# Optimization experiments

Hardware: AMD Instinct MI355X
Metric: run time of the kernel (lower is better)

The kernel has to match this reference:

```python
import jax, jax.numpy as jnp
import numpy as np

B = 256; SEED = 120; PRED = 24; D = 126; H = 1024
J = 14; JD = 9; HEADS = 4; DH = H // HEADS; SPLH = 128
PARENTS = (-1, -1, 0, 1, 2, 3, -1, 6, -1, -1, 8, 9, 10, 11)  # sparse SPL kinematic tree


def setup_inputs() -> dict:
    key = jax.random.key(0)
    ks = jax.random.split(key, 18)
    s = 0.02
    w = lambda k, shape: jax.random.normal(k, shape, dtype=jnp.float32) * s
    return {
        "poses": jax.random.normal(ks[0], (B, SEED + PRED, D), dtype=jnp.float32),
        "gru_Wih": w(ks[1], (3 * H, D)), "gru_Whh": w(ks[2], (3 * H, H)),
        "gru_bih": w(ks[3], (3 * H,)), "gru_bhh": w(ks[4], (3 * H,)),
        "pre_W": w(ks[5], (H, H)), "pre_b": w(ks[6], (H,)),
        "fp_W": w(ks[7], (H, D)), "fp_b": w(ks[8], (H,)),
        "inproj_W": w(ks[9], (3 * H, H)), "inproj_b": w(ks[10], (3 * H,)),
        "outproj_W": w(ks[11], (H, H)), "outproj_b": w(ks[12], (H,)),
        # per-joint SPL MLPs, stacked; root joints see zero-padded parent slot
        "spl_W1": w(ks[13], (J, SPLH, H + JD)), "spl_b1": w(ks[14], (J, SPLH)),
        "spl_W2": w(ks[15], (J, JD, SPLH)), "spl_b2": w(ks[16], (J, JD)),
    }


def _gru_cell(x, h, Wih, Whh, bih, bhh):
    gi = x @ Wih.T + bih
    gh = h @ Whh.T + bhh
    ir, iz, inn = jnp.split(gi, 3, axis=-1)
    hr, hz, hn = jnp.split(gh, 3, axis=-1)
    r = jax.nn.sigmoid(ir + hr)
    z = jax.nn.sigmoid(iz + hz)
    n = jnp.tanh(inn + r * hn)
    return (1.0 - z) * n + z * h


def _forward(poses, gru_Wih, gru_Whh, gru_bih, gru_bhh, pre_W, pre_b,
             fp_W, fp_b, inproj_W, inproj_b, outproj_W, outproj_b,
             spl_W1, spl_b1, spl_W2, spl_b2):
    input_seq = poses[:, :SEED]  # (B, T_in, D)
    # --- DCT motion attention (rFFT proxy) ---
    freq = jnp.fft.rfft(input_seq, axis=1).real          # (B, F, D), F = SEED//2+1
    feat = freq @ fp_W.T + fp_b                          # (B, F, H)
    qkv = feat @ inproj_W.T + inproj_b
    q, k, v = jnp.split(qkv, 3, axis=-1)
    hsplit = lambda t: t.reshape(t.shape[0], t.shape[1], HEADS, DH)
    q, k, v = hsplit(q), hsplit(k), hsplit(v)
    att = jax.nn.softmax(jnp.einsum('bqhd,bkhd->bhqk', q, k) / np.sqrt(DH).astype(np.float32), axis=-1)
    ctx = jnp.einsum('bhqk,bkhd->bqhd', att, v).reshape(feat.shape)
    attn_out = ctx @ outproj_W.T + outproj_b
    motion_ctx = attn_out.mean(axis=1)                   # (B, H)
    # --- GRU encode over seed ---
    h0 = jnp.zeros((poses.shape[0], H), dtype=poses.dtype)
    def enc(h, x):
        return _gru_cell(x, h, gru_Wih, gru_Whh, gru_bih, gru_bhh), None
    h, _ = jax.lax.scan(enc, h0, jnp.swapaxes(input_seq, 0, 1))
    x_last = input_seq[:, -1]
    # --- hierarchical SPL (sparse mode) ---
    def spl(hid):
        zero = jnp.zeros((hid.shape[0], JD), dtype=hid.dtype)
        preds = [None] * J
        for j in range(J):
            p = PARENTS[j]
            par = zero if p == -1 else preds[p]
            inp = jnp.concatenate([hid, par], axis=-1)   # (B, H+JD)
            hh = jax.nn.relu(inp @ spl_W1[j].T + spl_b1[j])
            preds[j] = jnp.tanh(hh @ spl_W2[j].T + spl_b2[j])
        return jnp.concatenate(preds, axis=-1)            # (B, J*JD)
    def dec(carry, _):
        x, hc = carry
        hc = _gru_cell(x, hc, gru_Wih, gru_Whh, gru_bih, gru_bhh)
        hid = jax.nn.relu(hc @ pre_W.T + pre_b) + motion_ctx
        x = x + spl(hid)
        return (x, hc), x
    _, ys = jax.lax.scan(dec, (x_last, h), None, length=PRED)
    return jnp.swapaxes(ys, 0, 1)                         # (B, PRED, D)


def reference(poses, gru_Wih, gru_Whh, gru_bih, gru_bhh, pre_W, pre_b,
              fp_W, fp_b, inproj_W, inproj_b, outproj_W, outproj_b,
              spl_W1, spl_b1, spl_W2, spl_b2):
    return _forward(poses, gru_Wih, gru_Whh, gru_bih, gru_bhh, pre_W, pre_b,
                    fp_W, fp_b, inproj_W, inproj_b, outproj_W, outproj_b,
                    spl_W1, spl_b1, spl_W2, spl_b2)
```

## Files before the change

kernel.cpp:

```cpp
#include <hip/hip_runtime.h>
#include <hip/hip_bf16.h>

typedef __hip_bfloat16 bf16;
typedef __attribute__((ext_vector_type(8))) short v8bf;
typedef __attribute__((ext_vector_type(16))) float f32x16;
typedef __attribute__((ext_vector_type(4))) float f32x4;
typedef unsigned long long ull;

#define B_    256
#define SEED_ 120
#define PRED_ 24
#define D_    126
#define H_    1024
#define F_    61
#define HEADS_ 4
#define DH_   256

#define GLD16(lds, g) __builtin_amdgcn_global_load_lds( \
    (const __attribute__((address_space(1))) unsigned int*)(g), \
    (__attribute__((address_space(3))) unsigned int*)(lds), 16, 0, 0)
#define VMWAIT(n) asm volatile("s_waitcnt vmcnt(" #n ")" ::: "memory")
#define BARRIER() do { __builtin_amdgcn_s_barrier(); __builtin_amdgcn_sched_barrier(0); } while(0)
#define AL(P) __hip_atomic_load((P), __ATOMIC_RELAXED, __HIP_MEMORY_SCOPE_AGENT)

__global__ void k_cos(float* cosT){
  int i = blockIdx.x*256 + threadIdx.x;
  if (i < F_*SEED_){
    int f = i / SEED_, t = i % SEED_;
    int ph = (f*t) % SEED_;
    cosT[i] = cosf(6.283185307179586f * (float)ph / (float)SEED_);
  }
}

__global__ __launch_bounds__(256) void k_dft2(const float* __restrict__ poses,
                      const float* __restrict__ cosT, bf16* __restrict__ freqbf){
  __shared__ float pl[SEED_*128];
  int b = blockIdx.x, tid = threadIdx.x;
  for (int i = tid; i < SEED_*D_; i += 256){
    int t = i / D_, d = i - t*D_;
    pl[t*128 + d] = poses[((size_t)b*(SEED_+PRED_) + t)*D_ + d];
  }
  __syncthreads();
  int d = tid & 127, f0 = tid >> 7;
  float acc[31];
  #pragma unroll
  for (int j = 0; j < 31; ++j) acc[j] = 0.f;
  for (int t = 0; t < SEED_; ++t){
    float v = pl[t*128 + d];
    #pragma unroll
    for (int j = 0; j < 31; ++j){
      int f = f0 + j*2;
      if (f < F_) acc[j] += cosT[f*SEED_ + t] * v;
    }
  }
  #pragma unroll
  for (int j = 0; j < 31; ++j){
    int f = f0 + j*2;
    if (f < F_) freqbf[((size_t)b*F_ + f)*128 + d] = __float2bfloat16(d < D_ ? acc[j] : 0.f);
  }
}

__global__ void c_poses(const float* __restrict__ poses, bf16* __restrict__ pk){
  int t = blockIdx.x, b = blockIdx.y, c = threadIdx.x;
  float v = (c < D_) ? poses[((size_t)b*(SEED_+PRED_) + t)*D_ + c] : 0.f;
  pk[(size_t)t*32768 + ((b>>5)*4 + (c>>5))*1024 + (b&31)*32 + (c&31)] = __float2bfloat16(v);
}

__global__ void c_xinit(const float* __restrict__ poses, float* __restrict__ x, bf16* __restrict__ xpk){
  int b = blockIdx.x, c = threadIdx.x;
  float v = (c < D_) ? poses[((size_t)b*(SEED_+PRED_) + (SEED_-1))*D_ + c] : 0.f;
  if (c < D_) x[b*D_ + c] = v;
  xpk[((b>>5)*4 + (c>>5))*1024 + (b&31)*32 + (c&31)] = __float2bfloat16(v);
}

__global__ void c_bf(const float* __restrict__ s, bf16* __restrict__ d, int n){
  int i = blockIdx.x*256 + threadIdx.x;
  if (i < n) d[i] = __float2bfloat16(s[i]);
}

__global__ void c_fpwt(const float* __restrict__ fpW, bf16* __restrict__ o){
  int dd = blockIdx.x;
  for (int k = threadIdx.x; k < H_; k += 256)
    o[(size_t)dd*H_ + k] = __float2bfloat16(dd < D_ ? fpW[(size_t)k*D_ + dd] : 0.f);
}

__global__ void c_wcat(const float* __restrict__ Wih, const float* __restrict__ Whh, bf16* __restrict__ o){
  int r = blockIdx.x;
  int jr; bool hasx, hash;
  if (r < 2048){ jr = r; hasx = true; hash = true; }
  else if (r < 3072){ jr = r; hasx = true; hash = false; }
  else { jr = r - 1024; hasx = false; hash = true; }
  bf16* row = o + (size_t)r*1152;
  for (int c = threadIdx.x; c < 1152; c += 256){
    float v = 0.f;
    if (c < D_) { if (hasx) v = Wih[(size_t)jr*D_ + c]; }
    else if (c >= 128){ if (hash) v = Whh[(size_t)jr*H_ + (c-128)]; }
    row[c] = __float2bfloat16(v);
  }
}

__global__ void c_bcat(const float* __restrict__ bih, const float* __restrict__ bhh, float* __restrict__ o){
  int r = blockIdx.x*256 + threadIdx.x;
  if (r >= 4096) return;
  float v;
  if (r < 2048) v = bih[r] + bhh[r];
  else if (r < 3072) v = bih[r];
  else v = bhh[r - 1024];
  o[r] = v;
}

__global__ __launch_bounds__(256) void c_wpk(const bf16* __restrict__ Wcat, bf16* __restrict__ Wpk){
  int chunk = blockIdx.x*4 + (threadIdx.x >> 6);
  int l = threadIdx.x & 63;
  int ks = chunk % 36; int t2 = chunk / 36; int g = t2 % 3; int ub = t2 / 3;
  int unit = ub*16 + (l & 15);
  bf16* dst = Wpk + (size_t)chunk*512 + l*8;
  #pragma unroll
  for (int e = 0; e < 8; ++e){
    int k = ks*32 + (l>>4)*8 + e;
    int row = (g==0) ? unit : (g==1) ? (1024+unit) : (k < 128 ? 2048+unit : 3072+unit);
    dst[e] = Wcat[(size_t)row*1152 + k];
  }
}

__global__ __launch_bounds__(256) void c_w1pk(const float* __restrict__ sW1, bf16* __restrict__ w1pk){
  int chunk = blockIdx.x*4 + (threadIdx.x >> 6);
  int l = threadIdx.x & 63;
  int ks = chunk & 31, ng = chunk >> 5;
  int unit = ng*16 + (l & 15);
  int j = unit >> 7, rr = unit & 127;
  bf16* dst = w1pk + (size_t)chunk*512 + l*8;
  #pragma unroll
  for (int e = 0; e < 8; ++e){
    int k = ks*32 + (l>>4)*8 + e;
    dst[e] = __float2bfloat16(sW1[((size_t)j*128 + rr)*1033 + k]);
  }
}

__global__ void c_w1par(const float* __restrict__ sW1, float* __restrict__ w1par){
  int i = blockIdx.x*256 + threadIdx.x;
  if (i < 14*9*128){
    int j = i / (9*128); int rem = i % (9*128); int ii = rem / 128; int th = rem % 128;
    w1par[i] = sW1[((size_t)(j*128 + th))*1033 + 1024 + ii];
  }
}

__global__ __launch_bounds__(256) void k_bc(const float* __restrict__ inW, const float* __restrict__ inb,
                     const float* __restrict__ fpb, float* __restrict__ bc){
  int wave = threadIdx.x >> 6, lane = threadIdx.x & 63;
  int r = blockIdx.x*4 + wave;
  const float4* row = (const float4*)(inW + (size_t)r*H_);
  const float4* fp4 = (const float4*)fpb;
  float s = 0.f;
  #pragma unroll
  for (int i = 0; i < 4; ++i){
    float4 a = row[lane + i*64];
    float4 b = fp4[lane + i*64];
    s += a.x*b.x + a.y*b.y + a.z*b.z + a.w*b.w;
  }
  #pragma unroll
  for (int off = 32; off; off >>= 1) s += __shfl_down(s, off);
  if (lane == 0) bc[r] = s + inb[r];
}

#define SLCP(QA, QB, KS, GACC) { \
  union { ull u[2]; v8bf v; } cc_; cc_.u[0]=(QA); cc_.u[1]=(QB); \
  v8bf a_ = cc_.v; \
  v8bf w0_ = *(const v8bf*)&Wl[(0*36+(KS))*512 + lane*8]; \
  v8bf w1_ = *(const v8bf*)&Wl[(1*36+(KS))*512 + lane*8]; \
  v8bf w2_ = *(const v8bf*)&Wl[(2*36+(KS))*512 + lane*8]; \
  aR = __builtin_amdgcn_mfma_f32_16x16x32_bf16(a_, w0_, aR, 0,0,0); \
  aZ = __builtin_amdgcn_mfma_f32_16x16x32_bf16(a_, w1_, aZ, 0,0,0); \
  GACC = __builtin_amdgcn_mfma_f32_16x16x32_bf16(a_, w2_, GACC, 0,0,0); }

#define LDHA(DA, DB, C) { \
  const ull* hp_ = (const ull*)(hs + hbase + (size_t)(C)*1024); \
  DA = AL(hp_); DB = AL(hp_+1); }

#define LDXP(DA, DB, TT, C) { \
  const ull* xp_ = (const ull*)(xpk + (size_t)(TT)*xstride + xbase + (size_t)(C)*1024); \
  DA = xp_[0]; DB = xp_[1]; }

__global__ __launch_bounds__(256) void gru_wave(
    const bf16* __restrict__ xpk, int xstride, int nsteps, int coop,
    const bf16* __restrict__ Wpk, const float* __restrict__ bcat,
    const float* __restrict__ hin_plain, float* __restrict__ hout_plain,
    bf16* __restrict__ hbplain,
    bf16* __restrict__ hpk0, bf16* __restrict__ hpk1,
    unsigned* __restrict__ prog)
{
  __shared__ bf16 Wl[3*36*512];
  const int tid = threadIdx.x, wave = tid >> 6, lane = tid & 63;
  const int ub = blockIdx.x & 63, q = blockIdx.x >> 6;
  const int u0 = ub*16;

  {
    const bf16* wsrc = Wpk + (size_t)ub*(3*36*512);
    #pragma unroll
    for (int i = 0; i < 27; ++i){
      int c = i*256 + tid;
      GLD16(&Wl[c*8], wsrc + (size_t)c*8);
    }
  }
  VMWAIT(0); BARRIER();

  const int la = lane & 15, lb = lane >> 4;
  const int r0 = q*64 + wave*16;
  const int rb = r0 >> 5, y = wave & 1;
  const int ucol = u0 + la;
  const float bR = bcat[ucol], bZ = bcat[1024+ucol], bI = bcat[2048+ucol], bN = bcat[3072+ucol];
  const size_t hbase = (size_t)rb*32768 + (size_t)y*512 + la*32 + lb*8;
  const size_t xbase = (size_t)rb*4096  + (size_t)y*512 + la*32 + lb*8;
  const size_t pwb = (size_t)rb*32768 + (size_t)(u0>>5)*1024 + (size_t)y*512 + (u0&16) + la;

  float hr[4];
  if (nsteps == 1){
    #pragma unroll
    for (int r = 0; r < 4; ++r) hr[r] = hin_plain[(size_t)(r0 + lb*4 + r)*1024 + ucol];
  } else {
    #pragma unroll
    for (int r = 0; r < 4; ++r) hr[r] = 0.f;
  }

  ull a0,a1,a2,a3,a4,a5,a6,a7,a8,a9,a10,a11;
  ull b0,b1,b2,b3,b4,b5,b6,b7,b8,b9,b10,b11;
  LDXP(a0,b0,0,0); LDXP(a1,b1,0,1); LDXP(a2,b2,0,2); LDXP(a3,b3,0,3);

  for (int t = 0; t < nsteps; ++t){
    if (coop && t > 0){
      if (wave == 0){
        unsigned v = AL(&prog[q*64 + lane]);
        while (__ballot(v >= (unsigned)t) != ~0ULL){
          __builtin_amdgcn_s_sleep(1);
          v = AL(&prog[q*64 + lane]);
        }
      }
      __syncthreads();
      __builtin_amdgcn_sched_barrier(0);
    }
    const bf16* hs = (t & 1) ? hpk1 : hpk0;
    LDHA(a4,b4,0) LDHA(a5,b5,1) LDHA(a6,b6,2) LDHA(a7,b7,3)
    LDHA(a8,b8,4) LDHA(a9,b9,5) LDHA(a10,b10,6) LDHA(a11,b11,7)

    f32x4 z4 = {0.f,0.f,0.f,0.f};
    f32x4 aR = z4, aZ = z4, aI = z4, aN = z4;

    SLCP(a0,b0,0,aI)  LDHA(a0,b0,8)
    SLCP(a1,b1,1,aI)  LDHA(a1,b1,9)
    SLCP(a2,b2,2,aI)  LDHA(a2,b2,10)
    SLCP(a3,b3,3,aI)  LDHA(a3,b3,11)
    SLCP(a4,b4,4,aN)  LDHA(a4,b4,12)
    SLCP(a5,b5,5,aN)  LDHA(a5,b5,13)
    SLCP(a6,b6,6,aN)  LDHA(a6,b6,14)
    SLCP(a7,b7,7,aN)  LDHA(a7,b7,15)
    SLCP(a8,b8,8,aN)  LDHA(a8,b8,16)
    SLCP(a9,b9,9,aN)  LDHA(a9,b9,17)
    SLCP(a10,b10,10,aN) LDHA(a10,b10,18)
    SLCP(a11,b11,11,aN) LDHA(a11,b11,19)
    SLCP(a0,b0,12,aN) LDHA(a0,b0,20)
    SLCP(a1,b1,13,aN) LDHA(a1,b1,21)
    SLCP(a2,b2,14,aN) LDHA(a2,b2,22)
    SLCP(a3,b3,15,aN) LDHA(a3,b3,23)
    SLCP(a4,b4,16,aN) LDHA(a4,b4,24)
    SLCP(a5,b5,17,aN) LDHA(a5,b5,25)
    SLCP(a6,b6,18,aN) LDHA(a6,b6,26)
    SLCP(a7,b7,19,aN) LDHA(a7,b7,27)
    SLCP(a8,b8,20,aN) LDHA(a8,b8,28)
    SLCP(a9,b9,21,aN) LDHA(a9,b9,29)
    SLCP(a10,b10,22,aN) LDHA(a10,b10,30)
    SLCP(a11,b11,23,aN) LDHA(a11,b11,31)
    SLCP(a0,b0,24,aN) LDXP(a0,b0,t+1,0)
    SLCP(a1,b1,25,aN) LDXP(a1,b1,t+1,1)
    SLCP(a2,b2,26,aN) LDXP(a2,b2,t+1,2)
    SLCP(a3,b3,27,aN) LDXP(a3,b3,t+1,3)
    SLCP(a4,b4,28,aN)
    SLCP(a5,b5,29,aN)
    SLCP(a6,b6,30,aN)
    SLCP(a7,b7,31,aN)
    SLCP(a8,b8,32,aN)
    SLCP(a9,b9,33,aN)
    SLCP(a10,b10,34,aN)
    SLCP(a11,b11,35,aN)

    bf16* hd = (t & 1) ? hpk0 : hpk1;
    const bool last = (t == nsteps-1);
    #pragma unroll
    for (int r = 0; r < 4; ++r){
      float rg = 1.f/(1.f + __expf(-(aR[r] + bR)));
      float zg = 1.f/(1.f + __expf(-(aZ[r] + bZ)));
      float ng = tanhf((aI[r] + bI) + rg*(aN[r] + bN));
      float hv = (1.f - zg)*ng + zg*hr[r];
      hr[r] = hv;
      bf16 hv16 = __float2bfloat16(hv);
      unsigned short hbits = *(unsigned short*)&hv16;
      __hip_atomic_store((unsigned short*)(hd + pwb + (size_t)(lb*4 + r)*32), hbits,
                         __ATOMIC_RELAXED, __HIP_MEMORY_SCOPE_AGENT);
      if (last){
        hout_plain[(size_t)(r0 + lb*4 + r)*1024 + ucol] = hv;
        if (hbplain) hbplain[(size_t)(r0 + lb*4 + r)*1024 + ucol] = __float2bfloat16(hv);
      }
    }
    if (coop && t + 1 < nsteps){
      VMWAIT(0);
      __syncthreads();
      if (tid == 0)
        __hip_atomic_store(&prog[q*64 + ub], (unsigned)(t+1), __ATOMIC_RELAXED, __HIP_MEMORY_SCOPE_AGENT);
    }
  }
}

__constant__ int LVJ[14] = {0,1,6,8,9, 2,3,7,10,11, 4,5,12,13};
__constant__ int LVO[4]  = {0,5,10,14};
__constant__ int PAR_[14] = {-1,-1,0,1,2,3,-1,6,-1,-1,8,9,10,11};

#define DGRL(S,C) { const ull* p_=(const ull*)(hspk + hbase + (size_t)(C)*1024); qa##S=AL(p_); qb##S=AL(p_+1); }
#define DGXL(S,C) { const ull* p_=(const ull*)(xpk + xbase + (size_t)(C)*1024); qa##S=AL(p_); qb##S=AL(p_+1); }
#define DGRC(S,KS,GACC) { union{ull u[2];v8bf v;}c_; c_.u[0]=qa##S;c_.u[1]=qb##S; v8bf a_=c_.v; \
  v8bf w0_=*(const v8bf*)&Wl[(KS)*512+lane*8]; \
  v8bf w1_=*(const v8bf*)&Wl[18432+(KS)*512+lane*8]; \
  v8bf w2_=*(const v8bf*)&Wl[36864+(KS)*512+lane*8]; \
  aR=__builtin_amdgcn_mfma_f32_16x16x32_bf16(a_,w0_,aR,0,0,0); \
  aZ=__builtin_amdgcn_mfma_f32_16x16x32_bf16(a_,w1_,aZ,0,0,0); \
  GACC=__builtin_amdgcn_mfma_f32_16x16x32_bf16(a_,w2_,GACC,0,0,0); }

__global__ __launch_bounds__(512) void gru_spl(
    const bf16* __restrict__ xpk, const bf16* __restrict__ Wpk,
    const float* __restrict__ bcat,
    const float* __restrict__ hin_plain, float* __restrict__ hout_plain,
    bf16* __restrict__ hbplain,
    const bf16* __restrict__ hspk, bf16* __restrict__ hdpk,
    const float* __restrict__ hhpre, const float* __restrict__ w1par,
    const float* __restrict__ sW2, const float* __restrict__ sb2,
    float* __restrict__ xcur, bf16* __restrict__ xpkw, float* __restrict__ out,
    int dt, unsigned* __restrict__ progS)
{
  __shared__ bf16 Wl[3*36*512];
  __shared__ float hhl[2][1792];
  __shared__ float preds_s[2][128];
  __shared__ float hh_s[128][2];
  const int tid = threadIdx.x, wave = tid >> 6, lane = tid & 63;
  const int bid = blockIdx.x;
  const int ub = bid >> 1, bs = bid & 1, u0 = ub*16;

  {
    const bf16* wsrc = Wpk + (size_t)ub*(3*36*512);
    #pragma unroll
    for (int i = 0; i < 14; ++i){ int c = i*512 + tid; if (c < 6912) GLD16(&Wl[c*8], wsrc + (size_t)c*8); }
  }

  const int b0s = bid*2, th = tid;
  if (dt > 0){
    for (int i = tid; i < 2*1792; i += 512){
      int bb = i / 1792, col = i - bb*1792;
      hhl[bb][col] = hhpre[(size_t)(b0s+bb)*1792 + col];
    }
    __syncthreads();
    for (int L = 0; L < 3; ++L){
      for (int ji = LVO[L]; ji < LVO[L+1]; ++ji){
        int j = LVJ[ji], p = PAR_[j];
        if (tid < 128){
          float a0s = hhl[0][j*128 + th], a1s = hhl[1][j*128 + th];
          if (p >= 0){
            #pragma unroll
            for (int ii = 0; ii < 9; ++ii){
              float w = w1par[(j*9 + ii)*128 + th];
              a0s += w * preds_s[0][p*9 + ii];
              a1s += w * preds_s[1][p*9 + ii];
            }
          }
          hh_s[th][0] = fmaxf(a0s, 0.f);
          hh_s[th][1] = fmaxf(a1s, 0.f);
        }
        __syncthreads();
        if (tid < 36){
          int pp = th >> 1, half = th & 1;
          int bb = pp/9, oi = pp%9;
          const float4* w4 = (const float4*)(sW2 + (size_t)(j*9 + oi)*128 + half*64);
          float s = 0.f;
          #pragma unroll
          for (int q2 = 0; q2 < 16; ++q2){
            float4 wv = w4[q2];
            s += hh_s[half*64 + q2*4 + 0][bb]*wv.x + hh_s[half*64 + q2*4 + 1][bb]*wv.y
               + hh_s[half*64 + q2*4 + 2][bb]*wv.z + hh_s[half*64 + q2*4 + 3][bb]*wv.w;
          }
          s += __shfl_xor(s, 1);
          if (half == 0) preds_s[bb][j*9 + oi] = tanhf(s + sb2[j*9 + oi]);
        }
        __syncthreads();
      }
    }
    if (tid < 128){
      for (int i = th; i < 2*D_; i += 128){
        int bb = i / D_, d = i % D_;
        int row = b0s + bb;
        size_t xi = (size_t)row*D_ + d;
        float v = xcur[xi] + preds_s[bb][d];
        xcur[xi] = v;
        bf16 v16 = __float2bfloat16(v);
        __hip_atomic_store((unsigned short*)(xpkw + ((size_t)(row>>5)*4 + (d>>5))*1024 + (row&31)*32 + (d&31)),
                           *(unsigned short*)&v16, __ATOMIC_RELAXED, __HIP_MEMORY_SCOPE_AGENT);
        out[((size_t)row*PRED_ + (dt-1))*D_ + d] = v;
      }
    }
    VMWAIT(0);
    __syncthreads();
    if (tid == 0)
      __hip_atomic_store(&progS[bid], (unsigned)dt, __ATOMIC_RELAXED, __HIP_MEMORY_SCOPE_AGENT);
  }

  VMWAIT(0); BARRIER();

  const int la = lane & 15, lb = lane >> 4;
  const int r0 = bs*128 + wave*16;
  const int rb = r0 >> 5, y = wave & 1;
  const int ucol = u0 + la;
  const float bR = bcat[ucol], bZ = bcat[1024+ucol], bI = bcat[2048+ucol], bN = bcat[3072+ucol];
  const size_t hbase = (size_t)rb*32768 + (size_t)y*512 + la*32 + lb*8;
  const size_t xbase = (size_t)rb*4096  + (size_t)y*512 + la*32 + lb*8;
  const size_t pwb = (size_t)rb*32768 + (size_t)(u0>>5)*1024 + (size_t)y*512 + (u0&16) + la;

  float hr[4];
  #pragma unroll
  for (int r = 0; r < 4; ++r) hr[r] = hin_plain[(size_t)(r0 + lb*4 + r)*1024 + ucol];

  ull qa0,qa1,qa2,qa3,qa4,qa5,qa6,qa7,qa8,qa9,qa10,qa11;
  ull qb0,qb1,qb2,qb3,qb4,qb5,qb6,qb7,qb8,qb9,qb10,qb11;

  DGRL(0,0) DGRL(1,1) DGRL(2,2) DGRL(3,3) DGRL(4,4) DGRL(5,5)
  DGRL(6,6) DGRL(7,7) DGRL(8,8) DGRL(9,9) DGRL(10,10) DGRL(11,11)
  f32x4 z4 = {0.f,0.f,0.f,0.f};
  f32x4 aR = z4, aZ = z4, aI = z4, aN = z4;
  DGRC(0,4,aN)  DGRL(0,12)
  DGRC(1,5,aN)  DGRL(1,13)
  DGRC(2,6,aN)  DGRL(2,14)
  DGRC(3,7,aN)  DGRL(3,15)
  DGRC(4,8,aN)  DGRL(4,16)
  DGRC(5,9,aN)  DGRL(5,17)
  DGRC(6,10,aN) DGRL(6,18)
  DGRC(7,11,aN) DGRL(7,19)
  DGRC(8,12,aN) DGRL(8,20)
  DGRC(9,13,aN) DGRL(9,21)
  DGRC(10,14,aN) DGRL(10,22)
  DGRC(11,15,aN) DGRL(11,23)
  DGRC(0,16,aN) DGRL(0,24)
  DGRC(1,17,aN) DGRL(1,25)
  DGRC(2,18,aN) DGRL(2,26)
  DGRC(3,19,aN) DGRL(3,27)
  DGRC(4,20,aN) DGRL(4,28)
  DGRC(5,21,aN) DGRL(5,29)
  DGRC(6,22,aN) DGRL(6,30)
  DGRC(7,23,aN) DGRL(7,31)
  DGRC(8,24,aN)
  DGRC(9,25,aN)
  DGRC(10,26,aN)
  DGRC(11,27,aN)
  DGRC(0,28,aN)
  DGRC(1,29,aN)
  DGRC(2,30,aN)
  DGRC(3,31,aN)
  DGRC(4,32,aN)
  DGRC(5,33,aN)
  DGRC(6,34,aN)
  DGRC(7,35,aN)
  if (dt > 0){
    if (wave == 0){
      unsigned v1 = AL(&progS[lane]), v2 = AL(&progS[64 + lane]);
      while (__ballot((v1 >= (unsigned)dt) && (v2 >= (unsigned)dt)) != ~0ULL){
        __builtin_amdgcn_s_sleep(2);
        v1 = AL(&progS[lane]); v2 = AL(&progS[64 + lane]);
      }
    }
    __syncthreads();
    __builtin_amdgcn_sched_barrier(0);
  }
  DGXL(8,0) DGXL(9,1) DGXL(10,2) DGXL(11,3)
  DGRC(8,0,aI)
  DGRC(9,1,aI)
  DGRC(10,2,aI)
  DGRC(11,3,aI)
  #pragma unroll
  for (int r = 0; r < 4; ++r){
    float rg = 1.f/(1.f + __expf(-(aR[r] + bR)));
    float zg = 1.f/(1.f + __expf(-(aZ[r] + bZ)));
    float ng = tanhf((aI[r] + bI) + rg*(aN[r] + bN));
    float hv = (1.f - zg)*ng + zg*hr[r];
    bf16 hv16 = __float2bfloat16(hv);
    __hip_atomic_store((unsigned short*)(hdpk + pwb + (size_t)(lb*4 + r)*32),
                       *(unsigned short*)&hv16, __ATOMIC_RELAXED, __HIP_MEMORY_SCOPE_AGENT);
    hout_plain[(size_t)(r0 + lb*4 + r)*1024 + ucol] = hv;
    hbplain[(size_t)(r0 + lb*4 + r)*1024 + ucol] = hv16;
  }
}

#define W1L(S,C) { const ull* p_=(const ull*)(hidpk + w1abase + (size_t)(C)*1024); \
  qa##S=AL(p_); qb##S=AL(p_+1); \
  bq##S = *(const uint4*)(w1b0 + (size_t)(C)*512 + lane*8); \
  br##S = *(const uint4*)(w1b1 + (size_t)(C)*512 + lane*8); }
#define W1C(S) { union{ull u[2];v8bf v;}x_; x_.u[0]=qa##S;x_.u[1]=qb##S; \
  union{uint4 q; v8bf v;}b0_,b1_; b0_.q=bq##S; b1_.q=br##S; \
  c0=__builtin_amdgcn_mfma_f32_16x16x32_bf16(x_.v,b0_.v,c0,0,0,0); \
  c1=__builtin_amdgcn_mfma_f32_16x16x32_bf16(x_.v,b1_.v,c1,0,0,0); }

__global__ __launch_bounds__(512) void gemm_pw(
    const bf16* __restrict__ hb, const bf16* __restrict__ prebf,
    const float* __restrict__ preb, const float* __restrict__ motion,
    bf16* __restrict__ hidpk, const bf16* __restrict__ w1pk,
    const float* __restrict__ sb1, float* __restrict__ hhpre,
    int dt, unsigned* __restrict__ progP)
{
  __shared__ bf16 As[3][64*64];
  __shared__ bf16 Bs[3][64*64];
  const int tid = threadIdx.x, wave = tid >> 6, lane = tid & 63;
  const int bid = blockIdx.x;
  const int la = lane & 15, lb = lane >> 4;

  if (bid < 64){
    const int m0 = (bid & 3)*64, n0 = (bid >> 2)*64;
    const int fr = lane & 31, kh = lane >> 5;
    const int wm = (wave >> 1)*32, wn = (wave & 1)*32;
    f32x16 acc = {0.f,0.f,0.f,0.f,0.f,0.f,0.f,0.f,0.f,0.f,0.f,0.f,0.f,0.f,0.f,0.f};

    auto STAGE = [&](int buf, int kt){
      if (tid < 256){
        #pragma unroll
        for (int q2 = 0; q2 < 2; ++q2){
          int idx = q2*256 + tid;
          int row = idx >> 3, cp = idx & 7, csw = cp ^ (row & 7);
          GLD16(&As[buf][idx*8], hb + (size_t)(m0+row)*1024 + kt*64 + csw*8);
        }
        #pragma unroll
        for (int q2 = 0; q2 < 2; ++q2){
          int idx = q2*256 + tid;
          int row = idx >> 3, cp = idx & 7, csw = cp ^ (row & 7);
          GLD16(&Bs[buf][idx*8], prebf + (size_t)(n0+row)*1024 + kt*64 + csw*8);
        }
      }
    };
    auto COMPUTE = [&](int buf){
      if (wave < 4){
        const bf16* Ab = &As[buf][0];
        const bf16* Bb = &Bs[buf][0];
        #pragma unroll
        for (int ks = 0; ks < 4; ++ks){
          int ca = ks*2 + kh;
          v8bf av = *(const v8bf*)&Ab[(wm+fr)*64 + ((ca ^ ((wm+fr)&7))*8)];
          v8bf bv = *(const v8bf*)&Bb[(wn+fr)*64 + ((ca ^ ((wn+fr)&7))*8)];
          acc = __builtin_amdgcn_mfma_f32_32x32x16_bf16(av, bv, acc, 0, 0, 0);
        }
      }
    };

    STAGE(0, 0); STAGE(1, 1);
    VMWAIT(4); BARRIER();
    for (int kt = 0; kt < 16; ++kt){
      if (kt + 2 < 16) STAGE((kt+2)%3, kt+2);
      COMPUTE(kt%3);
      if (kt + 2 < 16){ VMWAIT(4); BARRIER(); }
      else if (kt + 1 < 16){ VMWAIT(0); BARRIER(); }
    }
    if (wave < 4){
      const int col = n0 + wn + fr;
      const float bb2 = preb[col];
      #pragma unroll
      for (int r = 0; r < 16; ++r){
        int row = m0 + wm + (r&3) + 8*(r>>2) + 4*kh;
        float v = fmaxf(acc[r] + bb2, 0.f) + motion[(size_t)row*1024 + col];
        bf16 v16 = __float2bfloat16(v);
        __hip_atomic_store((unsigned short*)(hidpk + ((size_t)(row>>5)*32 + (col>>5))*1024 + (row&31)*32 + (col&31)),
                           *(unsigned short*)&v16, __ATOMIC_RELAXED, __HIP_MEMORY_SCOPE_AGENT);
      }
    }
    VMWAIT(0);
    __syncthreads();
    if (tid == 0)
      __hip_atomic_store(&progP[bid], (unsigned)(dt+1), __ATOMIC_RELAXED, __HIP_MEMORY_SCOPE_AGENT);
  }

  if (wave == 0){
    unsigned v = AL(&progP[lane]);
    while (__ballot(v >= (unsigned)(dt+1)) != ~0ULL){
      __builtin_amdgcn_s_sleep(2);
      v = AL(&progP[lane]);
    }
  }
  __syncthreads();
  __builtin_amdgcn_sched_barrier(0);

  const int mq = bid / 28, ng = bid % 28;
  const int mg = wave >> 1, nc = wave & 1;
  const int r0w = mq*64 + mg*16;
  const int w1rb = r0w >> 5, w1y = mg & 1;
  const size_t w1abase = (size_t)w1rb*32768 + (size_t)w1y*512 + la*32 + lb*8;
  const int ug0 = ng*4 + nc*2, ug1 = ug0 + 1;
  const bf16* w1b0 = w1pk + (size_t)ug0*(32*512);
  const bf16* w1b1 = w1pk + (size_t)ug1*(32*512);
  const float sb1a = sb1[ug0*16 + la];
  const float sb1b = sb1[ug1*16 + la];

  ull qa0,qa1,qa2,qa3,qa4,qa5;
  ull qb0,qb1,qb2,qb3,qb4,qb5;
  uint4 bq0,bq1,bq2,bq3,bq4,bq5;
  uint4 br0,br1,br2,br3,br4,br5;

  W1L(0,0) W1L(1,1) W1L(2,2) W1L(3,3) W1L(4,4) W1L(5,5)
  f32x4 c0 = {0.f,0.f,0.f,0.f}, c1 = c0;
  W1C(0) W1L(0,6)
  W1C(1) W1L(1,7)
  W1C(2) W1L(2,8)
  W1C(3) W1L(3,9)
  W1C(4) W1L(4,10)
  W1C(5) W1L(5,11)
  W1C(0) W1L(0,12)
  W1C(1) W1L(1,13)
  W1C(2) W1L(2,14)
  W1C(3) W1L(3,15)
  W1C(4) W1L(4,16)
  W1C(5) W1L(5,17)
  W1C(0) W1L(0,18)
  W1C(1) W1L(1,19)
  W1C(2) W1L(2,20)
  W1C(3) W1L(3,21)
  W1C(4) W1L(4,22)
  W1C(5) W1L(5,23)
  W1C(0) W1L(0,24)
  W1C(1) W1L(1,25)
  W1C(2) W1L(2,26)
  W1C(3) W1L(3,27)
  W1C(4) W1L(4,28)
  W1C(5) W1L(5,29)
  W1C(0) W1L(0,30)
  W1C(1) W1L(1,31)
  W1C(2)
  W1C(3)
  W1C(4)
  W1C(5)
  W1C(0)
  W1C(1)
  #pragma unroll
  for (int r = 0; r < 4; ++r){
    int row = r0w + lb*4 + r;
    hhpre[(size_t)row*1792 + ug0*16 + la] = c0[r] + sb1a;
    hhpre[(size_t)row*1792 + ug1*16 + la] = c1[r] + sb1b;
  }
}

__global__ __launch_bounds__(256) void gemm64(
    const bf16* __restrict__ Am, const bf16* __restrict__ Bm, int K,
    const float* __restrict__ bias, const float* __restrict__ addmat,
    float* __restrict__ C, bf16* __restrict__ Cbf, int N, int MODE)
{
  __shared__ bf16 As[3][64*64];
  __shared__ bf16 Bs[3][64*64];
  const int tid = threadIdx.x;
  const int wave = tid >> 6, lane = tid & 63;
  const int m0 = blockIdx.x*64, n0 = blockIdx.y*64;
  const int fr = lane & 31, kh = lane >> 5;
  const int wm = (wave >> 1)*32, wn = (wave & 1)*32;
  const int KT = K >> 6;

  f32x16 acc = {0.f,0.f,0.f,0.f,0.f,0.f,0.f,0.f,0.f,0.f,0.f,0.f,0.f,0.f,0.f,0.f};

  auto STAGE = [&](int buf, int kt){
    #pragma unroll
    for (int q = 0; q < 2; ++q){
      int idx = q*256 + tid;
      int row = idx >> 3, cp = idx & 7, csw = cp ^ (row & 7);
      GLD16(&As[buf][idx*8], Am + (size_t)(m0+row)*K + kt*64 + csw*8);
    }
    #pragma unroll
    for (int q = 0; q < 2; ++q){
      int idx = q*256 + tid;
      int row = idx >> 3, cp = idx & 7, csw = cp ^ (row & 7);
      GLD16(&Bs[buf][idx*8], Bm + (size_t)(n0+row)*K + kt*64 + csw*8);
    }
  };
  auto COMPUTE = [&](int buf){
    const bf16* Ab = &As[buf][0];
    const bf16* Bb = &Bs[buf][0];
    #pragma unroll
    for (int ks = 0; ks < 4; ++ks){
      int ca = ks*2 + kh;
      v8bf av = *(const v8bf*)&Ab[(wm+fr)*64 + ((ca ^ ((wm+fr)&7))*8)];
      v8bf bv = *(const v8bf*)&Bb[(wn+fr)*64 + ((ca ^ ((wn+fr)&7))*8)];
      acc = __builtin_amdgcn_mfma_f32_32x32x16_bf16(av, bv, acc, 0, 0, 0);
    }
  };

  STAGE(0, 0);
  if (KT > 1){ STAGE(1, 1); VMWAIT(4); } else { VMWAIT(0); }
  BARRIER();
  for (int kt = 0; kt < KT; ++kt){
    if (kt + 2 < KT) STAGE((kt+2)%3, kt+2);
    COMPUTE(kt%3);
    if (kt + 2 < KT){ VMWAIT(4); BARRIER(); }
    else if (kt + 1 < KT){ VMWAIT(0); BARRIER(); }
  }

  const int col = n0 + wn + fr;
  float bb = bias ? bias[col] : 0.f;
  #pragma unroll
  for (int r = 0; r < 16; ++r){
    int row = m0 + wm + (r&3) + 8*(r>>2) + 4*kh;
    float v = acc[r] + bb;
    if (MODE == 1) v = fmaxf(v, 0.f) + addmat[(size_t)row*N + col];
    if (C)   C[(size_t)row*N + col] = v;
    if (Cbf) Cbf[(size_t)row*N + col] = __float2bfloat16(v);
  }
}

__global__ __launch_bounds__(256) void k_attn(const bf16* __restrict__ qkv,
                                              bf16* __restrict__ ctxbf){
  __shared__ char smem[65536];
  bf16* qs = (bf16*)smem;
  bf16* ks = qs + 64*256;
  float* sc = (float*)smem;
  float* cs = (float*)(smem + 32768);
  const int h = blockIdx.x, b = blockIdx.y;
  const int tid = threadIdx.x, wave = tid >> 6, lane = tid & 63;
  const int fr = lane & 31, kh = lane >> 5;
  const int wm = (wave >> 1)*32, wn = (wave & 1)*32;

  #pragma unroll
  for (int i = 0; i < 8; ++i){
    int idx = i*256 + tid;
    int row = idx >> 5, cp = idx & 31, csw = cp ^ (row & 7);
    GLD16(&qs[idx*8], qkv + (size_t)(b*F_ + row)*3072 + h*DH_ + csw*8);
  }
  #pragma unroll
  for (int i = 0; i < 8; ++i){
    int idx = i*256 + tid;
    int row = idx >> 5, cp = idx & 31, csw = cp ^ (row & 7);
    GLD16(&ks[idx*8], qkv + (size_t)(b*F_ + row)*3072 + H_ + h*DH_ + csw*8);
  }
  __syncthreads();

  f32x16 acc = {0.f,0.f,0.f,0.f,0.f,0.f,0.f,0.f,0.f,0.f,0.f,0.f,0.f,0.f,0.f,0.f};
  #pragma unroll
  for (int i = 0; i < 16; ++i){
    int ca = i*2 + kh;
    v8bf av = *(const v8bf*)&qs[((wm+fr)*32 + (ca ^ ((wm+fr)&7)))*8];
    v8bf bv = *(const v8bf*)&ks[((wn+fr)*32 + (ca ^ ((wn+fr)&7)))*8];
    acc = __builtin_amdgcn_mfma_f32_32x32x16_bf16(av, bv, acc, 0, 0, 0);
  }
  __syncthreads();
  #pragma unroll
  for (int r = 0; r < 16; ++r){
    int row = wm + (r&3) + 8*(r>>2) + 4*kh;
    sc[row*65 + (wn+fr)] = acc[r]*0.0625f;
  }
  __syncthreads();
  if (tid < F_){
    float m = -1e30f;
    for (int k2 = 0; k2 < F_; ++k2) m = fmaxf(m, sc[tid*65+k2]);
    float s = 0.f;
    for (int k2 = 0; k2 < F_; ++k2){ float e = __expf(sc[tid*65+k2]-m); sc[tid*65+k2] = e; s += e; }
    float is = 1.f/s;
    for (int k2 = 0; k2 < F_; ++k2) sc[tid*65+k2] *= is;
  }
  __syncthreads();
  if (tid < F_){
    float s = 0.f;
    for (int r = 0; r < F_; ++r) s += sc[r*65+tid];
    cs[tid] = s;
  }
  __syncthreads();
  float a = 0.f;
  for (int k2 = 0; k2 < F_; ++k2){
    float v = __bfloat162float(qkv[(size_t)(b*F_+k2)*3072 + 2*H_ + h*DH_ + tid]);
    a += cs[k2]*v;
  }
  ctxbf[(size_t)b*H_ + h*DH_ + tid] = __float2bfloat16(a * (1.f/61.f));
}

__global__ __launch_bounds__(128) void spl_all(const float* __restrict__ hh_pre, const float* __restrict__ w1par,
                        const float* __restrict__ W2, const float* __restrict__ b2,
                        float* __restrict__ x, bf16* __restrict__ xpk,
                        float* __restrict__ out, int tstep){
  __shared__ float preds_s[4][128];
  __shared__ float hh_s[128][5];
  int b0 = blockIdx.x*4, t = threadIdx.x;
  for (int L = 0; L < 3; ++L){
    for (int ji = LVO[L]; ji < LVO[L+1]; ++ji){
      int j = LVJ[ji], p = PAR_[j];
      float acc[4];
      #pragma unroll
      for (int bb = 0; bb < 4; ++bb) acc[bb] = hh_pre[(size_t)(b0+bb)*1792 + j*128 + t];
      if (p >= 0){
        #pragma unroll
        for (int ii = 0; ii < 9; ++ii){
          float w = w1par[(j*9 + ii)*128 + t];
          #pragma unroll
          for (int bb = 0; bb < 4; ++bb) acc[bb] += w * preds_s[bb][p*9 + ii];
        }
      }
      #pragma unroll
      for (int bb = 0; bb < 4; ++bb) hh_s[t][bb] = fmaxf(acc[bb], 0.f);
      __syncthreads();
      if (t < 72){
        int pp = t >> 1, half = t & 1;
        int bb = pp/9, oi = pp%9;
        const float* w2r = W2 + (size_t)(j*9 + oi)*128 + half*64;
        float s = 0.f;
        #pragma unroll
        for (int tt = 0; tt < 64; ++tt) s += hh_s[half*64 + tt][bb] * w2r[tt];
        s += __shfl_xor(s, 1);
        if (half == 0) preds_s[bb][j*9 + oi] = tanhf(s + b2[j*9 + oi]);
      }
      __syncthreads();
    }
  }
  for (int i = t; i < 4*D_; i += 128){
    int bb = i / D_, d = i % D_;
    int row = b0 + bb;
    size_t xi = (size_t)row*D_ + d;
    float v = x[xi] + preds_s[bb][d];
    x[xi] = v;
    xpk[((row>>5)*4 + (d>>5))*1024 + (row&31)*32 + (d&31)] = __float2bfloat16(v);
    out[((size_t)row*PRED_ + tstep)*D_ + d] = v;
  }
}

extern "C" void kernel_launch(void* const* d_in, const int* in_sizes, int n_in,
                              void* d_out, int out_size, void* d_ws, size_t ws_size,
                              hipStream_t stream){
  (void)in_sizes; (void)n_in; (void)out_size; (void)ws_size;
  const float* poses = (const float*)d_in[0];
  const float* gWih  = (const float*)d_in[1];
  const float* gWhh  = (const float*)d_in[2];
  const float* gbih  = (const float*)d_in[3];
  const float* gbhh  = (const float*)d_in[4];
  const float* preW  = (const float*)d_in[5];
  const float* preb  = (const float*)d_in[6];
  const float* fpW   = (const float*)d_in[7];
  const float* fpb   = (const float*)d_in[8];
  const float* inW   = (const float*)d_in[9];
  const float* inb   = (const float*)d_in[10];
  const float* outW  = (const float*)d_in[11];
  const float* outb  = (const float*)d_in[12];
  const float* sW1   = (const float*)d_in[13];
  const float* sb1   = (const float*)d_in[14];
  const float* sW2   = (const float*)d_in[15];
  const float* sb2   = (const float*)d_in[16];
  float* out = (float*)d_out;

  char* w = (char*)d_ws;
  size_t off = 0;
  auto alloc = [&](size_t bytes)->char*{ char* p = w + off; off += (bytes + 255) & ~(size_t)255; return p; };
  float* cosT   = (float*)alloc(7320*4);
  float* bc     = (float*)alloc(3072*4);
  float* motion = (float*)alloc((size_t)256*1024*4);
  float* hA     = (float*)alloc((size_t)256*1024*4);
  float* hB     = (float*)alloc((size_t)256*1024*4);
  float* xcur   = (float*)alloc((size_t)256*126*4);
  float* hhpre  = (float*)alloc((size_t)256*1792*4);
  float* bcat   = (float*)alloc(4096*4);
  float* w1par  = (float*)alloc(14*9*128*4);
  unsigned* prog= (unsigned*)alloc(4096);
  bf16* posespk = (bf16*)alloc((size_t)121*32768*2);
  bf16* Wcat    = (bf16*)alloc((size_t)4096*1152*2);
  bf16* Wpk     = (bf16*)alloc((size_t)64*108*512*2);
  bf16* w1pk    = (bf16*)alloc((size_t)112*32*512*2);
  bf16* prebf   = (bf16*)alloc((size_t)1024*1024*2);
  bf16* outbf   = (bf16*)alloc((size_t)1024*1024*2);
  bf16* inbf    = (bf16*)alloc((size_t)3072*1024*2);
  bf16* fpwt    = (bf16*)alloc((size_t)128*1024*2);
  bf16* ctxbf   = (bf16*)alloc((size_t)256*1024*2);
  bf16* hpkA    = (bf16*)alloc((size_t)256*1024*2);
  bf16* hpkB    = (bf16*)alloc((size_t)256*1024*2);
  bf16* hbplain = (bf16*)alloc((size_t)256*1024*2);
  bf16* hidpk   = (bf16*)alloc((size_t)256*1024*2);
  bf16* xpk     = (bf16*)alloc((size_t)32768*2);
  bf16* Wcbf    = (bf16*)alloc((size_t)3072*128*2);
  bf16* freqbf  = (bf16*)alloc((size_t)B_*F_*128*2);
  bf16* qkvbf   = (bf16*)alloc((size_t)15680*3072*2);

  hipMemsetAsync(hpkA, 0, (size_t)256*1024*2, stream);
  hipMemsetAsync(prog, 0, 4096, stream);

  k_cos<<<29, 256, 0, stream>>>(cosT);
  k_dft2<<<B_, 256, 0, stream>>>(poses, cosT, freqbf);
  c_poses<<<dim3(SEED_, B_), 128, 0, stream>>>(poses, posespk);
  c_xinit<<<B_, 128, 0, stream>>>(poses, xcur, xpk);
  c_wcat<<<4096, 256, 0, stream>>>(gWih, gWhh, Wcat);
  c_bcat<<<16, 256, 0, stream>>>(gbih, gbhh, bcat);
  c_wpk<<<1728, 256, 0, stream>>>(Wcat, Wpk);
  c_w1pk<<<896, 256, 0, stream>>>(sW1, w1pk);
  c_w1par<<<63, 256, 0, stream>>>(sW1, w1par);
  c_bf<<<4096, 256, 0, stream>>>(preW, prebf, 1024*1024);
  c_bf<<<4096, 256, 0, stream>>>(outW, outbf, 1024*1024);
  c_bf<<<12288, 256, 0, stream>>>(inW, inbf, 3072*1024);
  c_fpwt<<<128, 256, 0, stream>>>(fpW, fpwt);
  k_bc<<<768, 256, 0, stream>>>(inW, inb, fpb, bc);

  gemm64<<<dim3(48, 2), 256, 0, stream>>>(inbf, fpwt, 1024, nullptr, nullptr, nullptr, Wcbf, 128, 0);
  gemm64<<<dim3(244, 48), 256, 0, stream>>>(freqbf, Wcbf, 128, bc, nullptr, nullptr, qkvbf, 3072, 0);
  k_attn<<<dim3(HEADS_, B_), 256, 0, stream>>>(qkvbf, ctxbf);
  gemm64<<<dim3(4, 16), 256, 0, stream>>>(ctxbf, outbf, 1024, outb, nullptr, motion, nullptr, 1024, 0);

  {
    const bf16* a0 = posespk; int a1 = 32768; int a2 = SEED_; int a3 = 1;
    const bf16* a4 = Wpk; const float* a5 = bcat;
    const float* a6 = hA; float* a7 = hA; bf16* a8 = nullptr;
    bf16* a9 = hpkA; bf16* a10 = hpkB; unsigned* a11 = prog;
    void* args[] = { &a0, &a1, &a2, &a3, &a4, &a5, &a6, &a7, &a8, &a9, &a10, &a11 };
    hipLaunchCooperativeKernel(reinterpret_cast<void*>(gru_wave), dim3(256), dim3(256),
                               args, 0, stream);
  }

  float* hc = hA;  float* hn = hB;
  bf16* hpc = hpkA; bf16* hpn = hpkB;
  unsigned* progS = prog + 256;
  unsigned* progP = prog + 384;

  for (int t = 0; t < PRED_; ++t){
    gru_spl<<<128, 512, 0, stream>>>(xpk, Wpk, bcat, hc, hn, hbplain, hpc, hpn,
                                     hhpre, w1par, sW2, sb2, xcur, xpk, out, t, progS);
    { float* tf = hc; hc = hn; hn = tf; bf16* tb = hpc; hpc = hpn; hpn = tb; }
    gemm_pw<<<112, 512, 0, stream>>>(hbplain, prebf, preb, motion, hidpk, w1pk, sb1, hhpre, t, progP);
  }
  spl_all<<<64, 128, 0, stream>>>(hhpre, w1par, sW2, sb2, xcur, xpk, out, PRED_-1);
}
```

Before: 2.781 ms.

## Split gru_spl into 256 blocks of 256 threads, one batch row each

The per-step GRU+SPL kernel is relaunched with 256 blocks of 256 threads instead of 128 blocks of 512. Each block now handles one batch row for the serial SPL tree and a quarter of the rows for the GRU MFMA tile. This spreads the latency-bound SPL work over more CUs and lets all four waves poll the progress flags. The cost is that each block still loads the full 16-unit weight slice into LDS, so there are twice as many weight loads in total, and there are more blocks to synchronise through the progress counters.

Measured after the change: 2.610 ms. 6.2% less time.

```diff
diff --git a/kernel.cpp b/kernel.cpp
--- a/kernel.cpp
+++ b/kernel.cpp
@@ -323,7 +323,7 @@
   aZ=__builtin_amdgcn_mfma_f32_16x16x32_bf16(a_,w1_,aZ,0,0,0); \
   GACC=__builtin_amdgcn_mfma_f32_16x16x32_bf16(a_,w2_,GACC,0,0,0); }
 
-__global__ __launch_bounds__(512) void gru_spl(
+__global__ __launch_bounds__(256) void gru_spl(
     const bf16* __restrict__ xpk, const bf16* __restrict__ Wpk,
     const float* __restrict__ bcat,
     const float* __restrict__ hin_plain, float* __restrict__ hout_plain,
@@ -335,72 +335,61 @@
     int dt, unsigned* __restrict__ progS)
 {
   __shared__ bf16 Wl[3*36*512];
-  __shared__ float hhl[2][1792];
-  __shared__ float preds_s[2][128];
-  __shared__ float hh_s[128][2];
+  __shared__ float hhl[1792];
+  __shared__ float preds_s[128];
+  __shared__ float hh_s[128];
   const int tid = threadIdx.x, wave = tid >> 6, lane = tid & 63;
   const int bid = blockIdx.x;
-  const int ub = bid >> 1, bs = bid & 1, u0 = ub*16;
+  const int ub = bid & 63, q = bid >> 6, u0 = ub*16;
 
   {
     const bf16* wsrc = Wpk + (size_t)ub*(3*36*512);
     #pragma unroll
-    for (int i = 0; i < 14; ++i){ int c = i*512 + tid; if (c < 6912) GLD16(&Wl[c*8], wsrc + (size_t)c*8); }
-  }
-
-  const int b0s = bid*2, th = tid;
+    for (int i = 0; i < 27; ++i){ int c = i*256 + tid; GLD16(&Wl[c*8], wsrc + (size_t)c*8); }
+  }
+
+  const int brow = bid, th = tid;
   if (dt > 0){
-    for (int i = tid; i < 2*1792; i += 512){
-      int bb = i / 1792, col = i - bb*1792;
-      hhl[bb][col] = hhpre[(size_t)(b0s+bb)*1792 + col];
-    }
+    for (int i = tid; i < 1792; i += 256) hhl[i] = hhpre[(size_t)brow*1792 + i];
     __syncthreads();
     for (int L = 0; L < 3; ++L){
       for (int ji = LVO[L]; ji < LVO[L+1]; ++ji){
         int j = LVJ[ji], p = PAR_[j];
         if (tid < 128){
-          float a0s = hhl[0][j*128 + th], a1s = hhl[1][j*128 + th];
+          float a0s = hhl[j*128 + th];
           if (p >= 0){
             #pragma unroll
-            for (int ii = 0; ii < 9; ++ii){
-              float w = w1par[(j*9 + ii)*128 + th];
-              a0s += w * preds_s[0][p*9 + ii];
-              a1s += w * preds_s[1][p*9 + ii];
-            }
+            for (int ii = 0; ii < 9; ++ii)
+              a0s += w1par[(j*9 + ii)*128 + th] * preds_s[p*9 + ii];
           }
-          hh_s[th][0] = fmaxf(a0s, 0.f);
-          hh_s[th][1] = fmaxf(a1s, 0.f);
+          hh_s[th] = fmaxf(a0s, 0.f);
         }
         __syncthreads();
-        if (tid < 36){
-          int pp = th >> 1, half = th & 1;
-          int bb = pp/9, oi = pp%9;
+        if (tid < 18){
+          int oi = th >> 1, half = th & 1;
           const float4* w4 = (const float4*)(sW2 + (size_t)(j*9 + oi)*128 + half*64);
           float s = 0.f;
           #pragma unroll
           for (int q2 = 0; q2 < 16; ++q2){
             float4 wv = w4[q2];
-            s += hh_s[half*64 + q2*4 + 0][bb]*wv.x + hh_s[half*64 + q2*4 + 1][bb]*wv.y
-               + hh_s[half*64 + q2*4 + 2][bb]*wv.z + hh_s[half*64 + q2*4 + 3][bb]*wv.w;
+            s += hh_s[half*64 + q2*4 + 0]*wv.x + hh_s[half*64 + q2*4 + 1]*wv.y
+               + hh_s[half*64 + q2*4 + 2]*wv.z + hh_s[half*64 + q2*4 + 3]*wv.w;
           }
           s += __shfl_xor(s, 1);
-          if (half == 0) preds_s[bb][j*9 + oi] = tanhf(s + sb2[j*9 + oi]);
+          if (half == 0) preds_s[j*9 + oi] = tanhf(s + sb2[j*9 + oi]);
         }
         __syncthreads();
       }
     }
-    if (tid < 128){
-      for (int i = th; i < 2*D_; i += 128){
-        int bb = i / D_, d = i % D_;
-        int row = b0s + bb;
-        size_t xi = (size_t)row*D_ + d;
-        float v = xcur[xi] + preds_s[bb][d];
-        xcur[xi] = v;
-        bf16 v16 = __float2bfloat16(v);
-        __hip_atomic_store((unsigned short*)(xpkw + ((size_t)(row>>5)*4 + (d>>5))*1024 + (row&31)*32 + (d&31)),
-                           *(unsigned short*)&v16, __ATOMIC_RELAXED, __HIP_MEMORY_SCOPE_AGENT);
-        out[((size_t)row*PRED_ + (dt-1))*D_ + d] = v;
-      }
+    if (tid < D_){
+      int d = tid;
+      size_t xi = (size_t)brow*D_ + d;
+      float v = xcur[xi] + preds_s[d];
+      xcur[xi] = v;
+      bf16 v16 = __float2bfloat16(v);
+      __hip_atomic_store((unsigned short*)(xpkw + ((size_t)(brow>>5)*4 + (d>>5))*1024 + (brow&31)*32 + (d&31)),
+                         *(unsigned short*)&v16, __ATOMIC_RELAXED, __HIP_MEMORY_SCOPE_AGENT);
+      out[((size_t)brow*PRED_ + (dt-1))*D_ + d] = v;
     }
     VMWAIT(0);
     __syncthreads();
@@ -411,7 +400,7 @@
   VMWAIT(0); BARRIER();
 
   const int la = lane & 15, lb = lane >> 4;
-  const int r0 = bs*128 + wave*16;
+  const int r0 = q*64 + wave*16;
   const int rb = r0 >> 5, y = wave & 1;
   const int ucol = u0 + la;
   const float bR = bcat[ucol], bZ = bcat[1024+ucol], bI = bcat[2048+ucol], bN = bcat[3072+ucol];
@@ -463,12 +452,10 @@
   DGRC(6,34,aN)
   DGRC(7,35,aN)
   if (dt > 0){
-    if (wave == 0){
-      unsigned v1 = AL(&progS[lane]), v2 = AL(&progS[64 + lane]);
-      while (__ballot((v1 >= (unsigned)dt) && (v2 >= (unsigned)dt)) != ~0ULL){
-        __builtin_amdgcn_s_sleep(2);
-        v1 = AL(&progS[lane]); v2 = AL(&progS[64 + lane]);
-      }
+    unsigned v = AL(&progS[wave*64 + lane]);
+    while (__ballot(v >= (unsigned)dt) != ~0ULL){
+      __builtin_amdgcn_s_sleep(2);
+      v = AL(&progS[wave*64 + lane]);
     }
     __syncthreads();
     __builtin_amdgcn_sched_barrier(0);
@@ -910,10 +897,10 @@
   float* hc = hA;  float* hn = hB;
   bf16* hpc = hpkA; bf16* hpn = hpkB;
   unsigned* progS = prog + 256;
-  unsigned* progP = prog + 384;
+  unsigned* progP = prog + 512;
 
   for (int t = 0; t < PRED_; ++t){
-    gru_spl<<<128, 512, 0, stream>>>(xpk, Wpk, bcat, hc, hn, hbplain, hpc, hpn,
+    gru_spl<<<256, 256, 0, stream>>>(xpk, Wpk, bcat, hc, hn, hbplain, hpc, hpn,
                                      hhpre, w1par, sW2, sb2, xcur, xpk, out, t, progS);
     { float* tf = hc; hc = hn; hn = tf; bf16* tb = hpc; hpc = hpn; hpn = tb; }
     gemm_pw<<<112, 512, 0, stream>>>(hbplain, prebf, preb, motion, hidpk, w1pk, sb1, hhpre, t, progP);
```
